# Performance work log

Hardware: AMD Instinct MI355X
Metric: run time of the kernel (lower is better)

The kernel has to match this reference:

```python
import jax, jax.numpy as jnp
import numpy as np
import math

B, S, D, H, L, FF, T = 2, 1024, 1024, 16, 8, 4096, 512
HD = D // H
EPS = 1e-5


def _ln(x, g, b):
    m = jnp.mean(x, axis=-1, keepdims=True)
    v = jnp.var(x, axis=-1, keepdims=True)
    return (x - m) * jax.lax.rsqrt(v + EPS) * g + b


def _rope(x, cos, sin):
    # x: [B,S,H,HD]; interleaved even/odd rotary as in _apply_rotary_emb_sincos
    xe, xo = x[..., 0::2], x[..., 1::2]
    c = cos[None, :, None, :]
    s = sin[None, :, None, :]
    return jnp.stack([xe * c - xo * s, xe * s + xo * c], axis=-1).reshape(x.shape)


def setup_inputs():
    key = jax.random.key(0)
    ks = iter(jax.random.split(key, 40))
    n = lambda shape, sc=0.02: jax.random.normal(next(ks), shape, jnp.float32) * sc
    return {
        "inputs_embeds": jax.random.normal(next(ks), (B, S, D), jnp.float32),
        "attention_mask": jnp.ones((B, 1, 1, S), jnp.float32),
        "time_step": jax.random.uniform(next(ks), (B,), jnp.float32),
        "wpe": n((S, D)),
        "ln1_g": jnp.ones((L, D)), "ln1_b": jnp.zeros((L, D)),
        "attn_w": n((L, D, 3 * D)), "attn_b": jnp.zeros((L, 3 * D)),
        "projw": n((L, D, D)), "projb": jnp.zeros((L, D)),
        "ln2_g": jnp.ones((L, D)), "ln2_b": jnp.zeros((L, D)),
        "fcw": n((L, D, FF)), "fcb": jnp.zeros((L, FF)),
        "pw2": n((L, FF, D)), "pb2": jnp.zeros((L, D)),
        "sst": n((L, 6, D), 1.0 / D ** 0.5),
        "te_w1": n((T, D)), "te_b1": jnp.zeros((D,)),
        "te_w2": n((D, D)), "te_b2": jnp.zeros((D,)),
        "ada_w": n((D, 6 * D)), "ada_b": jnp.zeros((6 * D,)),
        "lnf_g": jnp.ones((D,)), "lnf_b": jnp.zeros((D,)),
        "fsst": n((2, D), 1.0 / D ** 0.5),
        "out_w": n((D, D)), "out_b": jnp.zeros((D,)),
    }


def reference(inputs_embeds, attention_mask, time_step, wpe, ln1_g, ln1_b,
              attn_w, attn_b, projw, projb, ln2_g, ln2_b, fcw, fcb, pw2, pb2,
              sst, te_w1, te_b1, te_w2, te_b2, ada_w, ada_b, lnf_g, lnf_b,
              fsst, out_w, out_b):
    hs = inputs_embeds + wpe[:S][None]  # position embedding
    # rotary tables: [S, HD//2]
    half = HD // 2
    freqs = 1.0 / (10000.0 ** (jnp.arange(half, dtype=jnp.float32) * 2.0 / HD))
    ang = jnp.arange(S, dtype=jnp.float32)[:, None] * freqs[None]
    cos, sin = jnp.cos(ang), jnp.sin(ang)
    mask = (1.0 - attention_mask) * jnp.finfo(jnp.float32).min  # [B,1,1,S]
    # timestep embedding (flow_t_size=T, scale=1000, max_period=10000)
    halfT = T // 2
    tf = jnp.exp(-math.log(10000.0) * jnp.arange(halfT, dtype=jnp.float32) / halfT)
    targs = time_step[:, None] * tf[None] * 1000.0
    tproj = jnp.concatenate([jnp.cos(targs), jnp.sin(targs)], axis=-1)  # [B,T]
    emb = jax.nn.silu(tproj @ te_w1 + te_b1) @ te_w2 + te_b2  # [B,D]
    adaln = (jax.nn.silu(emb) @ ada_w + ada_b).reshape(B, 6, D)

    layer_params = dict(ln1_g=ln1_g, ln1_b=ln1_b, aw=attn_w, ab=attn_b,
                        pw=projw, pb=projb, ln2_g=ln2_g, ln2_b=ln2_b,
                        fw=fcw, fb=fcb, qw=pw2, qb=pb2, sst=sst)

    def block(h, p):
        mod = p["sst"][None] + adaln  # [B,6,D]
        sh1, sc1, g1, sh2, sc2, g2 = [mod[:, i:i + 1] for i in range(6)]
        res = h
        x = _ln(h, p["ln1_g"], p["ln1_b"]) * (1.0 + sc1) + sh1
        qkv = x @ p["aw"] + p["ab"]
        q, k, v = [t.reshape(B, S, H, HD) for t in jnp.split(qkv, 3, axis=-1)]
        q, k = _rope(q, cos, sin), _rope(k, cos, sin)
        scores = jnp.einsum("bqhd,bkhd->bhqk", q, k) / math.sqrt(HD) + mask
        attn = jax.nn.softmax(scores, axis=-1)
        o = jnp.einsum("bhqk,bkhd->bqhd", attn, v).reshape(B, S, D)
        o = o @ p["pw"] + p["pb"]
        h = o * g1 + res
        res = h
        x = _ln(h, p["ln2_g"], p["ln2_b"]) * (1.0 + sc2) + sh2
        x = jax.nn.gelu(x @ p["fw"] + p["fb"], approximate=True) @ p["qw"] + p["qb"]
        return x * g2 + res, None

    hs, _ = jax.lax.scan(block, hs, layer_params)
    fmod = fsst[None] + emb[:, None]  # [B,2,D]
    shift, scale = fmod[:, 0:1], fmod[:, 1:2]
    hs = _ln(hs, lnf_g, lnf_b) * (1.0 + scale) + shift
    return hs @ out_w + out_b
```

## Files before the change

kernel.cpp:

```cpp
#include <hip/hip_runtime.h>
#include <stdint.h>

typedef unsigned short u16;
typedef __attribute__((ext_vector_type(8))) short bf8_t;
typedef __attribute__((ext_vector_type(4))) float f4_t;

#define DEV static __device__ __forceinline__
#define MFMA16(a, b, c) __builtin_amdgcn_mfma_f32_16x16x32_bf16((a), (b), (c), 0, 0, 0)
#define GLDS(gp, lp) __builtin_amdgcn_global_load_lds((const __attribute__((address_space(1))) void*)(gp), \
                                                      (__attribute__((address_space(3))) void*)(lp), 16, 0, 0)

DEV u16 f2bf(float f) {
  union { float f; uint32_t u; } x; x.f = f;
  uint32_t r = x.u + 0x7FFFu + ((x.u >> 16) & 1u);
  return (u16)(r >> 16);
}

DEV void transpose_body(const float* __restrict__ W, u16* __restrict__ WT, int K, int N,
                        int n0, int k0, u16 (*tl)[66]) {
  const int t = threadIdx.x;
  const int tx = t & 15, ty = t >> 4;
  #pragma unroll
  for (int i = 0; i < 64; i += 16) {
    const float4 v = *(const float4*)&W[(long)(k0 + ty + i) * N + n0 + tx * 4];
    tl[tx * 4 + 0][ty + i] = f2bf(v.x);
    tl[tx * 4 + 1][ty + i] = f2bf(v.y);
    tl[tx * 4 + 2][ty + i] = f2bf(v.z);
    tl[tx * 4 + 3][ty + i] = f2bf(v.w);
  }
  __syncthreads();
  const int c = t & 15, r = t >> 4;
  #pragma unroll
  for (int i = 0; i < 64; i += 16) {
    const u16* p = &tl[r + i][c * 4];
    uint2 w;
    w.x = (uint32_t)p[0] | ((uint32_t)p[1] << 16);
    w.y = (uint32_t)p[2] | ((uint32_t)p[3] << 16);
    *(uint2*)&WT[(long)(n0 + r + i) * K + k0 + c * 4] = w;
  }
}

__global__ __launch_bounds__(256) void transpose_k(const float* __restrict__ W, u16* __restrict__ WT,
                                                   int K, int N) {
  __shared__ u16 tl[64][66];
  transpose_body(W, WT, K, N, blockIdx.x * 64, blockIdx.y * 64, tl);
}

__global__ __launch_bounds__(256)
void transpose4_k(const float* __restrict__ w0, u16* __restrict__ o0,
                  const float* __restrict__ w1, u16* __restrict__ o1,
                  const float* __restrict__ w2, u16* __restrict__ o2,
                  const float* __restrict__ w3, u16* __restrict__ o3) {
  __shared__ u16 tl[64][66];
  int bid = blockIdx.x;
  const float* W; u16* O; int K, N, nbx;
  if (bid < 768)        {             W = w0; O = o0; K = 1024; N = 3072; nbx = 48; }
  else if (bid < 1024)  { bid -= 768; W = w1; O = o1; K = 1024; N = 1024; nbx = 16; }
  else if (bid < 2048)  { bid -= 1024; W = w2; O = o2; K = 1024; N = 4096; nbx = 64; }
  else                  { bid -= 2048; W = w3; O = o3; K = 4096; N = 1024; nbx = 16; }
  transpose_body(W, O, K, N, (bid % nbx) * 64, (bid / nbx) * 64, tl);
}

enum { EPI_F32 = 0, EPI_GATE = 1, EPI_GELU = 2, EPI_RAW = 3 };

template <int BM, int EPI, int KS>
__global__ __launch_bounds__(256)
void gemm_bt(const u16* __restrict__ A, const u16* __restrict__ BT, const float* __restrict__ bias,
             float* outF, u16* outB, const float* gate, const float* res, int M, int N, int K) {
  constexpr int MI = BM / 32;
  __shared__ u16 sA[2][BM * 32];
  __shared__ u16 sB[2][128 * 32];
  const int tid = threadIdx.x, lane = tid & 63, wid = tid >> 6;
  const long rowBase = (long)blockIdx.x * BM;
  const long colBase = (long)blockIdx.y * 128;
  const int kz = (KS > 1) ? blockIdx.z : 0;
  const int kbeg = kz * (K / KS);
  const int wr = (wid >> 1) * (BM / 2), wc = (wid & 1) * 64;
  const int fr = lane & 15, kg = (lane >> 4) * 8;

  const f4_t zero = {0.0f, 0.0f, 0.0f, 0.0f};
  f4_t acc[MI][4];
  #pragma unroll
  for (int i = 0; i < MI; ++i)
    #pragma unroll
    for (int j = 0; j < 4; ++j) acc[i][j] = zero;

  const int sr = lane >> 2, scol = (lane & 3) * 8;
  const int c0 = wid * 2;
  const u16 *Ag0, *Ag1 = nullptr, *Bg0, *Bg1;
  int aoff0, aoff1 = 0, boff0, boff1;
  if constexpr (BM == 128) {
    Ag0 = A + (rowBase + c0 * 16 + sr) * (long)K + scol;
    Ag1 = A + (rowBase + c0 * 16 + 16 + sr) * (long)K + scol;
    aoff0 = (c0 * 16) * 32;
    aoff1 = (c0 * 16 + 16) * 32;
  } else {
    Ag0 = A + (rowBase + wid * 16 + sr) * (long)K + scol;
    aoff0 = (wid * 16) * 32;
  }
  Bg0 = BT + (colBase + c0 * 16 + sr) * (long)K + scol;
  Bg1 = BT + (colBase + c0 * 16 + 16 + sr) * (long)K + scol;
  boff0 = (c0 * 16) * 32;
  boff1 = (c0 * 16 + 16) * 32;

  auto stage = [&](int buf, int k0) {
    GLDS(Ag0 + k0, &sA[buf][aoff0]);
    if constexpr (BM == 128) GLDS(Ag1 + k0, &sA[buf][aoff1]);
// ... 9 lines not shown
    if (t + 1 < nk) stage(cur ^ 1, kbeg + (t + 1) * 32);
    bf8_t af[MI], bfv[4];
    #pragma unroll
    for (int m = 0; m < MI; ++m) af[m] = *(const bf8_t*)&sA[cur][(wr + m * 16 + fr) * 32 + kg];
    #pragma unroll
    for (int n = 0; n < 4; ++n) bfv[n] = *(const bf8_t*)&sB[cur][(wc + n * 16 + fr) * 32 + kg];
    #pragma unroll
    for (int m = 0; m < MI; ++m)
      #pragma unroll
      for (int n = 0; n < 4; ++n) acc[m][n] = MFMA16(af[m], bfv[n], acc[m][n]);
    __syncthreads();
    cur ^= 1;
  }

  const int r0 = (lane >> 4) * 4;
  #pragma unroll
  for (int m = 0; m < MI; ++m) {
    #pragma unroll
    for (int n = 0; n < 4; ++n) {
      const long col = colBase + wc + n * 16 + fr;
      const float bv = (EPI == EPI_RAW) ? 0.0f : bias[col];
      #pragma unroll
      for (int j = 0; j < 4; ++j) {
        const long row = rowBase + wr + m * 16 + r0 + j;
        float v = acc[m][n][j] + bv;
        if (EPI == EPI_F32) {
          outF[row * N + col] = v;
        } else if (EPI == EPI_RAW) {
          outF[((long)kz * M + row) * N + col] = v;
        } else if (EPI == EPI_GATE) {
          const int b = (int)(row >> 10);
          const float g = gate[(long)b * 6144 + col];
          outF[row * N + col] = v * g + res[row * N + col];
        } else {
          const float t = 0.7978845608028654f * (v + 0.044715f * v * v * v);
          const float e = __expf(2.0f * t);
          const float th = 1.0f - 2.0f / (e + 1.0f);
          outB[row * N + col] = f2bf(0.5f * v * (1.0f + th));
        }
      }
    }
  }
}

__global__ __launch_bounds__(256)
void ln_mod(const float* __restrict__ h, const float* __restrict__ gamma, const float* __restrict__ beta,
            const float* shp, const float* scp, int bstride, u16* __restrict__ xb) {
  const int row = blockIdx.x * 4 + (threadIdx.x >> 6);
  const int lane = threadIdx.x & 63;
  const int b = row >> 10;
  const long base = (long)row * 1024;
  f4_t x[4];
  float s = 0.0f;
  #pragma unroll
  for (int j = 0; j < 4; ++j) {
    x[j] = *(const f4_t*)&h[base + j * 256 + lane * 4];
    s += x[j][0] + x[j][1] + x[j][2] + x[j][3];
  }
  #pragma unroll
  for (int o = 32; o > 0; o >>= 1) s += __shfl_xor(s, o);
  const float mean = s * 0.0009765625f;
  float vs = 0.0f;
  #pragma unroll
  for (int j = 0; j < 4; ++j)
    #pragma unroll
    for (int e = 0; e < 4; ++e) { const float d = x[j][e] - mean; vs += d * d; }
// ... 37 lines not shown
    f4_t o;
    #pragma unroll
    for (int e = 0; e < 4; ++e) o[e] = (p[e] + q[e] + bv[e]) * gv[e] + r[e];
    *(f4_t*)&hs[base + col] = o;
    v[j] = o;
    s += o[0] + o[1] + o[2] + o[3];
  }
  #pragma unroll
  for (int o = 32; o > 0; o >>= 1) s += __shfl_xor(s, o);
  const float mean = s * 0.0009765625f;
  float vs = 0.0f;
  #pragma unroll
  for (int j = 0; j < 4; ++j)
    #pragma unroll
    for (int e = 0; e < 4; ++e) { const float d = v[j][e] - mean; vs += d * d; }
  #pragma unroll
  for (int o = 32; o > 0; o >>= 1) vs += __shfl_xor(vs, o);
  const float inv = rsqrtf(vs * 0.0009765625f + 1e-5f);
  #pragma unroll
  for (int j = 0; j < 4; ++j) {
    const int col = j * 256 + lane * 4;
    const f4_t gg = *(const f4_t*)&gamma[col];
    const f4_t bb = *(const f4_t*)&beta[col];
    const f4_t sh = *(const f4_t*)&shp[(long)b * bstride + col];
    const f4_t sc = *(const f4_t*)&scp[(long)b * bstride + col];
    union { u16 u[4]; uint2 v; } pk;
    #pragma unroll
    for (int e = 0; e < 4; ++e)
      pk.u[e] = f2bf(((v[j][e] - mean) * inv * gg[e] + bb[e]) * (1.0f + sc[e]) + sh[e]);
    *(uint2*)&xb[base + col] = pk.v;
  }
}

__global__ __launch_bounds__(256)
void rope_split(const float* __restrict__ qkv, const float* __restrict__ ct, const float* __restrict__ st,
                u16* __restrict__ qb, u16* __restrict__ kb) {
  const int row = blockIdx.x;
  const int b = row >> 10, s = row & 1023;
  const float* rp = qkv + (long)row * 3072;
  const int t = threadIdx.x;
  #pragma unroll
  for (int which = 0; which < 2; ++which) {
    const float* xp = rp + which * 1024;
    u16* op = which ? kb : qb;
    #pragma unroll
    for (int j = 0; j < 2; ++j) {
      const int p = t + j * 256;
      const int h = p >> 5, i = p & 31;
      const float2 xx = *(const float2*)&xp[h * 64 + 2 * i];
      const float c = ct[s * 32 + i], sn = st[s * 32 + i];
      const long base = (((long)(b * 16 + h)) * 1024 + s) * 64 + 2 * i;
      const uint32_t w = (uint32_t)f2bf(xx.x * c - xx.y * sn) |
                         ((uint32_t)f2bf(xx.x * sn + xx.y * c) << 16);
      *(uint32_t*)&op[base] = w;
    }
  }
}

__global__ __launch_bounds__(256)
void v_transpose(const float* __restrict__ qkv, u16* __restrict__ vt) {
  __shared__ u16 tl[64][66];
  const int s0 = blockIdx.x * 64;
  const int h = blockIdx.y, b = blockIdx.z;
  const int t = threadIdx.x;
  const int tx = t & 15, ty = t >> 4;
  #pragma unroll
  for (int i = 0; i < 64; i += 16) {
    const float4 v = *(const float4*)&qkv[(long)(b * 1024 + s0 + ty + i) * 3072 + 2048 + h * 64 + tx * 4];
    tl[tx * 4 + 0][ty + i] = f2bf(v.x);
    tl[tx * 4 + 1][ty + i] = f2bf(v.y);
    tl[tx * 4 + 2][ty + i] = f2bf(v.z);
    tl[tx * 4 + 3][ty + i] = f2bf(v.w);
  }
  __syncthreads();
  const int c = t & 15, r = t >> 4;
  #pragma unroll
  for (int i = 0; i < 64; i += 16) {
    const u16* p = &tl[r + i][c * 4];
    uint2 w;
    w.x = (uint32_t)p[0] | ((uint32_t)p[1] << 16);
    w.y = (uint32_t)p[2] | ((uint32_t)p[3] << 16);
    *(uint2*)&vt[((long)(b * 16 + h) * 64 + r + i) * 1024 + s0 + c * 4] = w;
  }
}

DEV void attn_body(bf8_t (&kcur)[4][2], bf8_t (&knxt)[4][2], const bf8_t (&qf)[2],
                   f4_t (&oacc)[4], float& m, float& psum, int kc,
                   const u16* __restrict__ Kp, const u16* __restrict__ Vt,
                   const float* smadd, u16* myP, int fr, int g) {
  const f4_t zero = {0.0f, 0.0f, 0.0f, 0.0f};
  bf8_t vf[4][2];
  #pragma unroll
  for (int dt = 0; dt < 4; ++dt)
    #pragma unroll
    for (int ks = 0; ks < 2; ++ks)
      vf[dt][ks] = *(const bf8_t*)&Vt[(long)(dt * 16 + fr) * 1024 + kc + ks * 32 + g * 8];
  f4_t st[4];
  #pragma unroll
  for (int kt = 0; kt < 4; ++kt) {
    st[kt] = MFMA16(kcur[kt][0], qf[0], zero);
    st[kt] = MFMA16(kcur[kt][1], qf[1], st[kt]);
  }
  {
    const int kn = (kc + 64) & 1023;
    #pragma unroll
    for (int kt = 0; kt < 4; ++kt)
      #pragma unroll
      for (int dh = 0; dh < 2; ++dh)
        knxt[kt][dh] = *(const bf8_t*)&Kp[(long)(kn + kt * 16 + fr) * 64 + dh * 32 + g * 8];
  }
  float p[4][4];
  float cm = -3.402823466e38f;
  #pragma unroll
  for (int kt = 0; kt < 4; ++kt) {
    const f4_t ma = *(const f4_t*)&smadd[kc + kt * 16 + g * 4];
    #pragma unroll
    for (int j = 0; j < 4; ++j) {
      p[kt][j] = st[kt][j] * 0.125f + ma[j];
      cm = fmaxf(cm, p[kt][j]);
    }
  }
  cm = fmaxf(cm, __shfl_xor(cm, 16));
  cm = fmaxf(cm, __shfl_xor(cm, 32));
  const float nm = fmaxf(m, cm);
  const float sc = __expf(m - nm);
  m = nm;
  float ls = 0.0f;
  #pragma unroll
  for (int kt = 0; kt < 4; ++kt)
    #pragma unroll
    for (int j = 0; j < 4; ++j) {
      p[kt][j] = __expf(p[kt][j] - nm);
      ls += p[kt][j];
    }
  psum = psum * sc + ls;
  #pragma unroll
  for (int dt = 0; dt < 4; ++dt)
    #pragma unroll
    for (int j = 0; j < 4; ++j) oacc[dt][j] *= sc;
  #pragma unroll
  for (int kt = 0; kt < 4; ++kt) {
    const int kb = kt * 2 + (g >> 1);
    uint2 w;
    w.x = (uint32_t)f2bf(p[kt][0]) | ((uint32_t)f2bf(p[kt][1]) << 16);
    w.y = (uint32_t)f2bf(p[kt][2]) | ((uint32_t)f2bf(p[kt][3]) << 16);
    *(uint2*)&myP[(kb * 16 + fr) * 8 + (g & 1) * 4] = w;
  }
  bf8_t pa0 = *(const bf8_t*)&myP[(g * 16 + fr) * 8];
  bf8_t pa1 = *(const bf8_t*)&myP[((4 + g) * 16 + fr) * 8];
  #pragma unroll
  for (int dt = 0; dt < 4; ++dt) {
    oacc[dt] = MFMA16(vf[dt][0], pa0, oacc[dt]);
    oacc[dt] = MFMA16(vf[dt][1], pa1, oacc[dt]);
  }
}

__global__ __launch_bounds__(64)
void attn_k(const u16* __restrict__ qb, const u16* __restrict__ kb, const u16* __restrict__ vt,
            const float* __restrict__ amask, u16* __restrict__ ob) {
  __shared__ float smadd[1024];
  __shared__ u16 pl[1024];
  const int q0 = blockIdx.x * 16;
  const int h = blockIdx.y, b = blockIdx.z;
  const long bh = b * 16 + h;
  const int lane = threadIdx.x;
  const int fr = lane & 15, g = lane >> 4;

  #pragma unroll
  for (int i = 0; i < 4; ++i) {
    const int e = (lane + i * 64) * 4;
    const f4_t am = *(const f4_t*)&amask[b * 1024 + e];
    f4_t md;
    #pragma unroll
    for (int j = 0; j < 4; ++j) md[j] = (1.0f - am[j]) * -3.402823466e38f;
    *(f4_t*)&smadd[e] = md;
  }

  const u16* Q = qb + (bh * 1024 + q0) * 64;
  const u16* Kp = kb + bh * 1024 * 64;
  const u16* Vt = vt + bh * 64 * 1024;

  bf8_t qf[2];
  qf[0] = *(const bf8_t*)&Q[fr * 64 + g * 8];
  qf[1] = *(const bf8_t*)&Q[fr * 64 + 32 + g * 8];

  const f4_t zero = {0.0f, 0.0f, 0.0f, 0.0f};
  f4_t oacc[4];
  #pragma unroll
  for (int dt = 0; dt < 4; ++dt) oacc[dt] = zero;
  float m = -1e30f, psum = 0.0f;

  bf8_t kfA[4][2], kfB[4][2];
  #pragma unroll
  for (int kt = 0; kt < 4; ++kt)
    #pragma unroll
    for (int dh = 0; dh < 2; ++dh)
      kfA[kt][dh] = *(const bf8_t*)&Kp[(long)(kt * 16 + fr) * 64 + dh * 32 + g * 8];

  for (int kc = 0; kc < 1024; kc += 128) {
    attn_body(kfA, kfB, qf, oacc, m, psum, kc, Kp, Vt, smadd, pl, fr, g);
    attn_body(kfB, kfA, qf, oacc, m, psum, kc + 64, Kp, Vt, smadd, pl, fr, g);
  }

  float ts = psum + __shfl_xor(psum, 16);
  ts += __shfl_xor(ts, 32);
  const float inv = 1.0f / ts;
  const long qrow = (long)b * 1024 + q0 + fr;
  #pragma unroll
  for (int dt = 0; dt < 4; ++dt) {
    union { u16 u[4]; uint2 v; } pk;
    #pragma unroll
    for (int j = 0; j < 4; ++j) pk.u[j] = f2bf(oacc[dt][j] * inv);
    *(uint2*)&ob[qrow * 1024 + h * 64 + dt * 16 + g * 4] = pk.v;
  }
}

__global__ void rope_tables(float* ct, float* st) {
  const int i = blockIdx.x * 256 + threadIdx.x;
  const int s = i >> 5, k = i & 31;
  const float freq = __expf(-9.210340371976184f * (float)(2 * k) / 64.0f);
  const float a = (float)s * freq;
  ct[i] = cosf(a);
  st[i] = sinf(a);
}

__global__ void init_hs(const float* __restrict__ e, const float* __restrict__ wpe, float* __restrict__ hs) {
  const long i = (long)blockIdx.x * 256 + threadIdx.x;
  float4 a = ((const float4*)e)[i];
  const float4 w = ((const float4*)wpe)[i & 262143];
  a.x += w.x; a.y += w.y; a.z += w.z; a.w += w.w;
  ((float4*)hs)[i] = a;
}

__global__ void time_proj_k(const float* __restrict__ ts, float* __restrict__ tproj) {
  const int j = blockIdx.x * 256 + threadIdx.x;
  const int b = blockIdx.y;
  const float tf = __expf(-9.210340371976184f * (float)(j & 255) / 256.0f);
  const float a = ts[b] * tf * 1000.0f;
  tproj[b * 512 + j] = (j < 256) ? cosf(a) : sinf(a);
}

__global__ __launch_bounds__(256)
void time_mlp1(const float* __restrict__ tproj, const float* __restrict__ w1,
               const float* __restrict__ b1, float* __restrict__ h1) {
  __shared__ float red[8][32];
  const int dl = threadIdx.x & 31, sl = threadIdx.x >> 5;
  const int d = blockIdx.x * 32 + dl, b = blockIdx.y;
  float acc = 0.0f;
  for (int j = sl * 64; j < sl * 64 + 64; ++j) acc += tproj[b * 512 + j] * w1[(long)j * 1024 + d];
  red[sl][dl] = acc;
  __syncthreads();
  if (threadIdx.x < 32) {
    const int dd = blockIdx.x * 32 + threadIdx.x;
    float a = b1[dd];
    #pragma unroll
    for (int s = 0; s < 8; ++s) a += red[s][threadIdx.x];
    h1[b * 1024 + dd] = a / (1.0f + __expf(-a));
  }
}

__global__ __launch_bounds__(256)
void time_mlp2(const float* __restrict__ h1, const float* __restrict__ w2,
               const float* __restrict__ b2, float* __restrict__ emb) {
  __shared__ float red[8][32];
  const int dl = threadIdx.x & 31, sl = threadIdx.x >> 5;
  const int d = blockIdx.x * 32 + dl, b = blockIdx.y;
  float acc = 0.0f;
  for (int j = sl * 128; j < sl * 128 + 128; ++j) acc += h1[b * 1024 + j] * w2[(long)j * 1024 + d];
  red[sl][dl] = acc;
  __syncthreads();
  if (threadIdx.x < 32) {
    const int dd = blockIdx.x * 32 + threadIdx.x;
    float a = b2[dd];
    #pragma unroll
    for (int s = 0; s < 8; ++s) a += red[s][threadIdx.x];
    emb[b * 1024 + dd] = a;
  }
}

__global__ void silu_k(const float* __restrict__ in, float* __restrict__ out, int n) {
  const int i = blockIdx.x * 256 + threadIdx.x;
  if (i < n) { const float v = in[i]; out[i] = v / (1.0f + __expf(-v)); }
}

__global__ void adaln_part(const float* __restrict__ se, const float* __restrict__ aw,
                           float* __restrict__ part) {
  const int j = blockIdx.x * 256 + threadIdx.x;
  const int b = blockIdx.y, kz = blockIdx.z;
  float acc = 0.0f;
  for (int k = kz * 128; k < kz * 128 + 128; ++k) acc += se[b * 1024 + k] * aw[(long)k * 6144 + j];
  part[((long)kz * 2 + b) * 6144 + j] = acc;
}

__global__ void adaln_reduce(const float* __restrict__ part, const float* __restrict__ ab,
                             float* __restrict__ adaln) {
  const int j = blockIdx.x * 256 + threadIdx.x;
  const int b = blockIdx.y;
  float acc = ab[j];
  #pragma unroll
  for (int kz = 0; kz < 8; ++kz) acc += part[((long)kz * 2 + b) * 6144 + j];
  adaln[b * 6144 + j] = acc;
}

__global__ void build_mods(const float* __restrict__ sst, const float* __restrict__ adaln,
                           const float* __restrict__ fsst, const float* __restrict__ emb,
                           float* __restrict__ modAll, float* __restrict__ fmod) {
  const int i = blockIdx.x * 256 + threadIdx.x;
  if (i < 98304) {
    const int d = i & 1023;
    const int rest = i >> 10;
    const int slot = rest % 6;
    const int t2 = rest / 6;
    const int bb = t2 & 1, l = t2 >> 1;
    modAll[i] = sst[(long)(l * 6 + slot) * 1024 + d] + adaln[bb * 6144 + slot * 1024 + d];
  } else if (i < 98304 + 4096) {
    const int j = i - 98304;
    const int d = j & 1023;
    const int slot = (j >> 10) & 1;
    const int bb = j >> 11;
    fmod[j] = fsst[slot * 1024 + d] + emb[bb * 1024 + d];
  }
}

// ... 8 lines not shown
  const float* ln1_b  = (const float*)d_in[5];
  const float* attn_w = (const float*)d_in[6];
  const float* attn_b = (const float*)d_in[7];
  const float* projw  = (const float*)d_in[8];
  const float* projb  = (const float*)d_in[9];
  const float* ln2_g  = (const float*)d_in[10];
  const float* ln2_b  = (const float*)d_in[11];
  const float* fcw    = (const float*)d_in[12];
  const float* fcb    = (const float*)d_in[13];
  const float* pw2    = (const float*)d_in[14];
  const float* pb2    = (const float*)d_in[15];
  const float* sst    = (const float*)d_in[16];
  const float* te_w1  = (const float*)d_in[17];
  const float* te_b1  = (const float*)d_in[18];
  const float* te_w2  = (const float*)d_in[19];
  const float* te_b2  = (const float*)d_in[20];
  const float* ada_w  = (const float*)d_in[21];
  const float* ada_b  = (const float*)d_in[22];
  const float* lnf_g  = (const float*)d_in[23];
  const float* lnf_b  = (const float*)d_in[24];
  const float* fsst   = (const float*)d_in[25];
  const float* out_w  = (const float*)d_in[26];
  const float* out_b  = (const float*)d_in[27];
  float* out = (float*)d_out;
  (void)in_sizes; (void)n_in; (void)out_size; (void)ws_size;

  char* wsb = (char*)d_ws;
  size_t off = 0;
  auto alloc = [&](size_t bytes) -> void* {
    void* p = wsb + off;
    off += (bytes + 255) & ~(size_t)255;
    return p;
  };
  u16* wtA = (u16*)alloc(3072ll * 1024 * 2);
  u16* wtP = (u16*)alloc(1024ll * 1024 * 2);
  u16* wtF = (u16*)alloc(4096ll * 1024 * 2);
  u16* wtQ = (u16*)alloc(1024ll * 4096 * 2);
  u16* wtO = (u16*)alloc(1024ll * 1024 * 2);
  float* hs   = (float*)alloc(2048ll * 1024 * 4);
  float* qkv  = (float*)alloc(2048ll * 3072 * 4);
  u16*   ffb  = (u16*)qkv;
  float* part = (float*)alloc(2ll * 2048 * 1024 * 4);
  u16* xb = (u16*)alloc(2048ll * 1024 * 2);
  u16* qb = (u16*)alloc(2048ll * 1024 * 2);
  u16* kb = (u16*)alloc(2048ll * 1024 * 2);
  u16* vt = (u16*)alloc(2048ll * 1024 * 2);
  u16* ob = (u16*)alloc(2048ll * 1024 * 2);
  float* ct    = (float*)alloc(32768 * 4);
  float* st    = (float*)alloc(32768 * 4);
  float* tproj = (float*)alloc(2 * 512 * 4);
  float* h1    = (float*)alloc(2 * 1024 * 4);
  float* emb   = (float*)alloc(2 * 1024 * 4);
  float* se    = (float*)alloc(2 * 1024 * 4);
  float* adaln = (float*)alloc(2 * 6144 * 4);
  float* modAll = (float*)alloc(8ll * 2 * 6 * 1024 * 4);
  float* fmod   = (float*)alloc(2 * 2 * 1024 * 4);

  rope_tables<<<128, 256, 0, stream>>>(ct, st);
  init_hs<<<2048, 256, 0, stream>>>(inp_emb, wpe, hs);
  time_proj_k<<<dim3(2, 2), 256, 0, stream>>>(tstep, tproj);
  time_mlp1<<<dim3(32, 2), 256, 0, stream>>>(tproj, te_w1, te_b1, h1);
  time_mlp2<<<dim3(32, 2), 256, 0, stream>>>(h1, te_w2, te_b2, emb);
  silu_k<<<8, 256, 0, stream>>>(emb, se, 2048);
  adaln_part<<<dim3(24, 2, 8), 256, 0, stream>>>(se, ada_w, part);
  adaln_reduce<<<dim3(24, 2), 256, 0, stream>>>(part, ada_b, adaln);
  build_mods<<<400, 256, 0, stream>>>(sst, adaln, fsst, emb, modAll, fmod);
  transpose_k<<<dim3(16, 16), 256, 0, stream>>>(out_w, wtO, 1024, 1024);

  ln_mod<<<512, 256, 0, stream>>>(hs, ln1_g, ln1_b, modAll + 0 * 1024, modAll + 1 * 1024, 6144, xb);

  for (int l = 0; l < 8; ++l) {
    const float* ml = modAll + (long)l * 12288;
    transpose4_k<<<3072, 256, 0, stream>>>(attn_w + (long)l * 1024 * 3072, wtA,
                                           projw + (long)l * 1024 * 1024, wtP,
                                           fcw + (long)l * 1024 * 4096, wtF,
                                           pw2 + (long)l * 4096 * 1024, wtQ);

    gemm_bt<128, EPI_F32, 1><<<dim3(16, 24), 256, 0, stream>>>(xb, wtA, attn_b + l * 3072,
                                                               qkv, nullptr, nullptr, nullptr, 2048, 3072, 1024);
    rope_split<<<2048, 256, 0, stream>>>(qkv, ct, st, qb, kb);
    v_transpose<<<dim3(16, 16, 2), 256, 0, stream>>>(qkv, vt);
    attn_k<<<dim3(64, 16, 2), 64, 0, stream>>>(qb, kb, vt, amask, ob);
    gemm_bt<64, EPI_GATE, 1><<<dim3(32, 8), 256, 0, stream>>>(ob, wtP, projb + l * 1024,
                                                              hs, nullptr, ml + 2 * 1024, hs, 2048, 1024, 1024);
    ln_mod<<<512, 256, 0, stream>>>(hs, ln2_g + l * 1024, ln2_b + l * 1024,
                                    ml + 3 * 1024, ml + 4 * 1024, 6144, xb);
    gemm_bt<128, EPI_GELU, 1><<<dim3(16, 32), 256, 0, stream>>>(xb, wtF, fcb + l * 4096,
                                                                nullptr, ffb, nullptr, nullptr, 2048, 4096, 1024);
    gemm_bt<128, EPI_RAW, 2><<<dim3(16, 8, 2), 256, 0, stream>>>(ffb, wtQ, nullptr,
                                                                 part, nullptr, nullptr, nullptr, 2048, 1024, 4096);
    if (l < 7) {
      const float* mln = modAll + (long)(l + 1) * 12288;
      reduce_gate_ln<<<512, 256, 0, stream>>>(part, pb2 + l * 1024, ml + 5 * 1024, hs,
                                              ln1_g + (l + 1) * 1024, ln1_b + (l + 1) * 1024,
                                              mln + 0 * 1024, mln + 1 * 1024, 6144, xb);
    } else {
      reduce_gate_ln<<<512, 256, 0, stream>>>(part, pb2 + l * 1024, ml + 5 * 1024, hs,
                                              lnf_g, lnf_b, fmod + 0, fmod + 1024, 2048, xb);
    }
  }

  gemm_bt<64, EPI_F32, 1><<<dim3(32, 8), 256, 0, stream>>>(xb, wtO, out_b,
                                                           out, nullptr, nullptr, nullptr, 2048, 1024, 1024);
}
```

Baseline: 1.826 ms.

## Split attention over KV halves, batch weight transposes, fuse small prologue kernels

Attention now splits the key/value range into two halves per query tile, which doubles the grid size. A new combine kernel merges the two partial results using their saved max and sum values. All eight layers' weight transposes now run in one launch before the layer loop rather than once per layer. RoPE and the V transpose are fused into one kernel, and time_proj and silu are folded into their consumer kernels. The cost is extra fp32 partial-output traffic and one more kernel per layer, plus larger buffers to hold the transposed weights for every layer.

```diff
diff --git a/kernel.cpp b/kernel.cpp
--- a/kernel.cpp
+++ b/kernel.cpp
@@ -47,17 +47,19 @@
 }
 
 __global__ __launch_bounds__(256)
-void transpose4_k(const float* __restrict__ w0, u16* __restrict__ o0,
-                  const float* __restrict__ w1, u16* __restrict__ o1,
-                  const float* __restrict__ w2, u16* __restrict__ o2,
-                  const float* __restrict__ w3, u16* __restrict__ o3) {
+void transpose_all(const float* __restrict__ attn_w, u16* __restrict__ wtA,
+                   const float* __restrict__ projw, u16* __restrict__ wtP,
+                   const float* __restrict__ fcw, u16* __restrict__ wtF,
+                   const float* __restrict__ pw2, u16* __restrict__ wtQ) {
   __shared__ u16 tl[64][66];
   int bid = blockIdx.x;
+  const int l = bid / 3072;
+  bid -= l * 3072;
   const float* W; u16* O; int K, N, nbx;
-  if (bid < 768)        {             W = w0; O = o0; K = 1024; N = 3072; nbx = 48; }
-  else if (bid < 1024)  { bid -= 768; W = w1; O = o1; K = 1024; N = 1024; nbx = 16; }
-  else if (bid < 2048)  { bid -= 1024; W = w2; O = o2; K = 1024; N = 4096; nbx = 64; }
-  else                  { bid -= 2048; W = w3; O = o3; K = 4096; N = 1024; nbx = 16; }
+  if (bid < 768)        {             W = attn_w + (long)l * 3145728; O = wtA + (long)l * 3145728; K = 1024; N = 3072; nbx = 48; }
+  else if (bid < 1024)  { bid -= 768; W = projw + (long)l * 1048576; O = wtP + (long)l * 1048576; K = 1024; N = 1024; nbx = 16; }
+  else if (bid < 2048)  { bid -= 1024; W = fcw + (long)l * 4194304; O = wtF + (long)l * 4194304; K = 1024; N = 4096; nbx = 64; }
+  else                  { bid -= 2048; W = pw2 + (long)l * 4194304; O = wtQ + (long)l * 4194304; K = 4096; N = 1024; nbx = 16; }
   transpose_body(W, O, K, N, (bid % nbx) * 64, (bid / nbx) * 64, tl);
 }
 
@@ -252,59 +254,52 @@
 }
 
 __global__ __launch_bounds__(256)
-void rope_split(const float* __restrict__ qkv, const float* __restrict__ ct, const float* __restrict__ st,
-                u16* __restrict__ qb, u16* __restrict__ kb) {
-  const int row = blockIdx.x;
-  const int b = row >> 10, s = row & 1023;
-  const float* rp = qkv + (long)row * 3072;
-  const int t = threadIdx.x;
-  #pragma unroll
-  for (int which = 0; which < 2; ++which) {
-    const float* xp = rp + which * 1024;
-    u16* op = which ? kb : qb;
-    #pragma unroll
-    for (int j = 0; j < 2; ++j) {
-      const int p = t + j * 256;
-      const int h = p >> 5, i = p & 31;
-      const float2 xx = *(const float2*)&xp[h * 64 + 2 * i];
-      const float c = ct[s * 32 + i], sn = st[s * 32 + i];
-      const long base = (((long)(b * 16 + h)) * 1024 + s) * 64 + 2 * i;
-      const uint32_t w = (uint32_t)f2bf(xx.x * c - xx.y * sn) |
-                         ((uint32_t)f2bf(xx.x * sn + xx.y * c) << 16);
-      *(uint32_t*)&op[base] = w;
-    }
-  }
-}
-
-__global__ __launch_bounds__(256)
-void v_transpose(const float* __restrict__ qkv, u16* __restrict__ vt) {
+void rope_v(const float* __restrict__ qkv, const float* __restrict__ ct, const float* __restrict__ st,
+            u16* __restrict__ qb, u16* __restrict__ kb, u16* __restrict__ vt) {
   __shared__ u16 tl[64][66];
   const int s0 = blockIdx.x * 64;
   const int h = blockIdx.y, b = blockIdx.z;
+  const long bh = b * 16 + h;
   const int t = threadIdx.x;
+
+  const int i = t & 31, r0 = t >> 5;
+  #pragma unroll
+  for (int which = 0; which < 2; ++which) {
+    u16* op = which ? kb : qb;
+    #pragma unroll
+    for (int it = 0; it < 8; ++it) {
+      const int s = s0 + r0 + it * 8;
+      const float2 xx = *(const float2*)&qkv[(long)(b * 1024 + s) * 3072 + which * 1024 + h * 64 + 2 * i];
+      const float c = ct[s * 32 + i], sn = st[s * 32 + i];
+      const uint32_t w = (uint32_t)f2bf(xx.x * c - xx.y * sn) |
+                         ((uint32_t)f2bf(xx.x * sn + xx.y * c) << 16);
+      *(uint32_t*)&op[(bh * 1024 + s) * 64 + 2 * i] = w;
+    }
+  }
+
   const int tx = t & 15, ty = t >> 4;
   #pragma unroll
-  for (int i = 0; i < 64; i += 16) {
-    const float4 v = *(const float4*)&qkv[(long)(b * 1024 + s0 + ty + i) * 3072 + 2048 + h * 64 + tx * 4];
-    tl[tx * 4 + 0][ty + i] = f2bf(v.x);
-    tl[tx * 4 + 1][ty + i] = f2bf(v.y);
-    tl[tx * 4 + 2][ty + i] = f2bf(v.z);
-    tl[tx * 4 + 3][ty + i] = f2bf(v.w);
+  for (int i2 = 0; i2 < 64; i2 += 16) {
+    const float4 v = *(const float4*)&qkv[(long)(b * 1024 + s0 + ty + i2) * 3072 + 2048 + h * 64 + tx * 4];
+    tl[tx * 4 + 0][ty + i2] = f2bf(v.x);
+    tl[tx * 4 + 1][ty + i2] = f2bf(v.y);
+    tl[tx * 4 + 2][ty + i2] = f2bf(v.z);
+    tl[tx * 4 + 3][ty + i2] = f2bf(v.w);
   }
   __syncthreads();
-  const int c = t & 15, r = t >> 4;
-  #pragma unroll
-  for (int i = 0; i < 64; i += 16) {
-    const u16* p = &tl[r + i][c * 4];
+  const int c2 = t & 15, r2 = t >> 4;
+  #pragma unroll
+  for (int i2 = 0; i2 < 64; i2 += 16) {
+    const u16* p = &tl[r2 + i2][c2 * 4];
     uint2 w;
     w.x = (uint32_t)p[0] | ((uint32_t)p[1] << 16);
     w.y = (uint32_t)p[2] | ((uint32_t)p[3] << 16);
-    *(uint2*)&vt[((long)(b * 16 + h) * 64 + r + i) * 1024 + s0 + c * 4] = w;
+    *(uint2*)&vt[(bh * 64 + r2 + i2) * 1024 + s0 + c2 * 4] = w;
   }
 }
 
 DEV void attn_body(bf8_t (&kcur)[4][2], bf8_t (&knxt)[4][2], const bf8_t (&qf)[2],
-                   f4_t (&oacc)[4], float& m, float& psum, int kc,
+                   f4_t (&oacc)[4], float& m, float& psum, int kc, int kv0,
                    const u16* __restrict__ Kp, const u16* __restrict__ Vt,
                    const float* smadd, u16* myP, int fr, int g) {
   const f4_t zero = {0.0f, 0.0f, 0.0f, 0.0f};
@@ -321,7 +316,7 @@
     st[kt] = MFMA16(kcur[kt][1], qf[1], st[kt]);
   }
   {
-    const int kn = (kc + 64) & 1023;
+    const int kn = kv0 + ((kc - kv0 + 64) & 511);
     #pragma unroll
     for (int kt = 0; kt < 4; ++kt)
       #pragma unroll
@@ -375,12 +370,14 @@
 }
 
 __global__ __launch_bounds__(64)
-void attn_k(const u16* __restrict__ qb, const u16* __restrict__ kb, const u16* __restrict__ vt,
-            const float* __restrict__ amask, u16* __restrict__ ob) {
+void attn_part(const u16* __restrict__ qb, const u16* __restrict__ kb, const u16* __restrict__ vt,
+               const float* __restrict__ amask, float* __restrict__ pO, float2* __restrict__ pml) {
   __shared__ float smadd[1024];
   __shared__ u16 pl[1024];
   const int q0 = blockIdx.x * 16;
-  const int h = blockIdx.y, b = blockIdx.z;
+  const int h = blockIdx.y;
+  const int bz = blockIdx.z, b = bz >> 1, half = bz & 1;
+  const int kv0 = half * 512;
   const long bh = b * 16 + h;
   const int lane = threadIdx.x;
   const int fr = lane & 15, g = lane >> 4;
@@ -414,24 +411,41 @@
   for (int kt = 0; kt < 4; ++kt)
     #pragma unroll
     for (int dh = 0; dh < 2; ++dh)
-      kfA[kt][dh] = *(const bf8_t*)&Kp[(long)(kt * 16 + fr) * 64 + dh * 32 + g * 8];
-
-  for (int kc = 0; kc < 1024; kc += 128) {
-    attn_body(kfA, kfB, qf, oacc, m, psum, kc, Kp, Vt, smadd, pl, fr, g);
-    attn_body(kfB, kfA, qf, oacc, m, psum, kc + 64, Kp, Vt, smadd, pl, fr, g);
+      kfA[kt][dh] = *(const bf8_t*)&Kp[(long)(kv0 + kt * 16 + fr) * 64 + dh * 32 + g * 8];
+
+  for (int kc = kv0; kc < kv0 + 512; kc += 128) {
+    attn_body(kfA, kfB, qf, oacc, m, psum, kc, kv0, Kp, Vt, smadd, pl, fr, g);
+    attn_body(kfB, kfA, qf, oacc, m, psum, kc + 64, kv0, Kp, Vt, smadd, pl, fr, g);
   }
 
   float ts = psum + __shfl_xor(psum, 16);
   ts += __shfl_xor(ts, 32);
-  const float inv = 1.0f / ts;
   const long qrow = (long)b * 1024 + q0 + fr;
-  #pragma unroll
-  for (int dt = 0; dt < 4; ++dt) {
-    union { u16 u[4]; uint2 v; } pk;
-    #pragma unroll
-    for (int j = 0; j < 4; ++j) pk.u[j] = f2bf(oacc[dt][j] * inv);
-    *(uint2*)&ob[qrow * 1024 + h * 64 + dt * 16 + g * 4] = pk.v;
-  }
+  float* pOh = pO + (long)half * 2048 * 1024;
+  #pragma unroll
+  for (int dt = 0; dt < 4; ++dt)
+    *(f4_t*)&pOh[qrow * 1024 + h * 64 + dt * 16 + g * 4] = oacc[dt];
+  if (g == 0)
+    pml[(((long)half * 2 + b) * 16 + h) * 1024 + q0 + fr] = make_float2(m, ts);
+}
+
+__global__ __launch_bounds__(256)
+void attn_combine(const float* __restrict__ pO, const float2* __restrict__ pml, u16* __restrict__ ob) {
+  const int row = blockIdx.x;
+  const int b = row >> 10, s = row & 1023;
+  const int t = threadIdx.x;
+  const int h = t >> 4;
+  const float2 a0 = pml[(((long)0 * 2 + b) * 16 + h) * 1024 + s];
+  const float2 a1 = pml[(((long)1 * 2 + b) * 16 + h) * 1024 + s];
+  const float M = fmaxf(a0.x, a1.x);
+  const float w0 = __expf(a0.x - M), w1 = __expf(a1.x - M);
+  const float inv = 1.0f / (a0.y * w0 + a1.y * w1);
+  const f4_t o0 = *(const f4_t*)&pO[(long)row * 1024 + t * 4];
+  const f4_t o1 = *(const f4_t*)&pO[2048ll * 1024 + (long)row * 1024 + t * 4];
+  union { u16 u[4]; uint2 v; } pk;
+  #pragma unroll
+  for (int j = 0; j < 4; ++j) pk.u[j] = f2bf((o0[j] * w0 + o1[j] * w1) * inv);
+  *(uint2*)&ob[(long)row * 1024 + t * 4] = pk.v;
 }
 
 __global__ void rope_tables(float* ct, float* st) {
@@ -451,22 +465,20 @@
   ((float4*)hs)[i] = a;
 }
 
-__global__ void time_proj_k(const float* __restrict__ ts, float* __restrict__ tproj) {
-  const int j = blockIdx.x * 256 + threadIdx.x;
-  const int b = blockIdx.y;
-  const float tf = __expf(-9.210340371976184f * (float)(j & 255) / 256.0f);
-  const float a = ts[b] * tf * 1000.0f;
-  tproj[b * 512 + j] = (j < 256) ? cosf(a) : sinf(a);
-}
-
-__global__ __launch_bounds__(256)
-void time_mlp1(const float* __restrict__ tproj, const float* __restrict__ w1,
+__global__ __launch_bounds__(256)
+void time_mlp1(const float* __restrict__ ts, const float* __restrict__ w1,
                const float* __restrict__ b1, float* __restrict__ h1) {
   __shared__ float red[8][32];
   const int dl = threadIdx.x & 31, sl = threadIdx.x >> 5;
   const int d = blockIdx.x * 32 + dl, b = blockIdx.y;
+  const float tsv = ts[b];
   float acc = 0.0f;
-  for (int j = sl * 64; j < sl * 64 + 64; ++j) acc += tproj[b * 512 + j] * w1[(long)j * 1024 + d];
+  for (int j = sl * 64; j < sl * 64 + 64; ++j) {
+    const float tf = __expf(-9.210340371976184f * (float)(j & 255) / 256.0f);
+    const float a = tsv * tf * 1000.0f;
+    const float val = (j < 256) ? cosf(a) : sinf(a);
+    acc += val * w1[(long)j * 1024 + d];
+  }
   red[sl][dl] = acc;
   __syncthreads();
   if (threadIdx.x < 32) {
@@ -497,17 +509,15 @@
   }
 }
 
-__global__ void silu_k(const float* __restrict__ in, float* __restrict__ out, int n) {
-  const int i = blockIdx.x * 256 + threadIdx.x;
-  if (i < n) { const float v = in[i]; out[i] = v / (1.0f + __expf(-v)); }
-}
-
-__global__ void adaln_part(const float* __restrict__ se, const float* __restrict__ aw,
+__global__ void adaln_part(const float* __restrict__ emb, const float* __restrict__ aw,
                            float* __restrict__ part) {
   const int j = blockIdx.x * 256 + threadIdx.x;
   const int b = blockIdx.y, kz = blockIdx.z;
   float acc = 0.0f;
-  for (int k = kz * 128; k < kz * 128 + 128; ++k) acc += se[b * 1024 + k] * aw[(long)k * 6144 + j];
+  for (int k = kz * 128; k < kz * 128 + 128; ++k) {
+    const float e = emb[b * 1024 + k];
+    acc += (e / (1.0f + __expf(-e))) * aw[(long)k * 6144 + j];
+  }
   part[((long)kz * 2 + b) * 6144 + j] = acc;
 }
 
@@ -582,15 +592,17 @@
     off += (bytes + 255) & ~(size_t)255;
     return p;
   };
-  u16* wtA = (u16*)alloc(3072ll * 1024 * 2);
-  u16* wtP = (u16*)alloc(1024ll * 1024 * 2);
-  u16* wtF = (u16*)alloc(4096ll * 1024 * 2);
-  u16* wtQ = (u16*)alloc(1024ll * 4096 * 2);
+  u16* wtA = (u16*)alloc(8ll * 3072 * 1024 * 2);
+  u16* wtP = (u16*)alloc(8ll * 1024 * 1024 * 2);
+  u16* wtF = (u16*)alloc(8ll * 4096 * 1024 * 2);
+  u16* wtQ = (u16*)alloc(8ll * 1024 * 4096 * 2);
   u16* wtO = (u16*)alloc(1024ll * 1024 * 2);
   float* hs   = (float*)alloc(2048ll * 1024 * 4);
   float* qkv  = (float*)alloc(2048ll * 3072 * 4);
   u16*   ffb  = (u16*)qkv;
   float* part = (float*)alloc(2ll * 2048 * 1024 * 4);
+  float* pO   = (float*)alloc(2ll * 2048 * 1024 * 4);
+  float2* pml = (float2*)alloc(2ll * 2 * 16 * 1024 * 8);
   u16* xb = (u16*)alloc(2048ll * 1024 * 2);
   u16* qb = (u16*)alloc(2048ll * 1024 * 2);
   u16* kb = (u16*)alloc(2048ll * 1024 * 2);
@@ -598,46 +610,38 @@
   u16* ob = (u16*)alloc(2048ll * 1024 * 2);
   float* ct    = (float*)alloc(32768 * 4);
   float* st    = (float*)alloc(32768 * 4);
-  float* tproj = (float*)alloc(2 * 512 * 4);
   float* h1    = (float*)alloc(2 * 1024 * 4);
   float* emb   = (float*)alloc(2 * 1024 * 4);
-  float* se    = (float*)alloc(2 * 1024 * 4);
   float* adaln = (float*)alloc(2 * 6144 * 4);
   float* modAll = (float*)alloc(8ll * 2 * 6 * 1024 * 4);
   float* fmod   = (float*)alloc(2 * 2 * 1024 * 4);
 
   rope_tables<<<128, 256, 0, stream>>>(ct, st);
   init_hs<<<2048, 256, 0, stream>>>(inp_emb, wpe, hs);
-  time_proj_k<<<dim3(2, 2), 256, 0, stream>>>(tstep, tproj);
-  time_mlp1<<<dim3(32, 2), 256, 0, stream>>>(tproj, te_w1, te_b1, h1);
+  time_mlp1<<<dim3(32, 2), 256, 0, stream>>>(tstep, te_w1, te_b1, h1);
   time_mlp2<<<dim3(32, 2), 256, 0, stream>>>(h1, te_w2, te_b2, emb);
-  silu_k<<<8, 256, 0, stream>>>(emb, se, 2048);
-  adaln_part<<<dim3(24, 2, 8), 256, 0, stream>>>(se, ada_w, part);
+  adaln_part<<<dim3(24, 2, 8), 256, 0, stream>>>(emb, ada_w, part);
   adaln_reduce<<<dim3(24, 2), 256, 0, stream>>>(part, ada_b, adaln);
   build_mods<<<400, 256, 0, stream>>>(sst, adaln, fsst, emb, modAll, fmod);
   transpose_k<<<dim3(16, 16), 256, 0, stream>>>(out_w, wtO, 1024, 1024);
+  transpose_all<<<8 * 3072, 256, 0, stream>>>(attn_w, wtA, projw, wtP, fcw, wtF, pw2, wtQ);
 
   ln_mod<<<512, 256, 0, stream>>>(hs, ln1_g, ln1_b, modAll + 0 * 1024, modAll + 1 * 1024, 6144, xb);
 
   for (int l = 0; l < 8; ++l) {
     const float* ml = modAll + (long)l * 12288;
-    transpose4_k<<<3072, 256, 0, stream>>>(attn_w + (long)l * 1024 * 3072, wtA,
-                                           projw + (long)l * 1024 * 1024, wtP,
-                                           fcw + (long)l * 1024 * 4096, wtF,
-                                           pw2 + (long)l * 4096 * 1024, wtQ);
-
-    gemm_bt<128, EPI_F32, 1><<<dim3(16, 24), 256, 0, stream>>>(xb, wtA, attn_b + l * 3072,
+    gemm_bt<128, EPI_F32, 1><<<dim3(16, 24), 256, 0, stream>>>(xb, wtA + (long)l * 3145728, attn_b + l * 3072,
                                                                qkv, nullptr, nullptr, nullptr, 2048, 3072, 1024);
-    rope_split<<<2048, 256, 0, stream>>>(qkv, ct, st, qb, kb);
-    v_transpose<<<dim3(16, 16, 2), 256, 0, stream>>>(qkv, vt);
-    attn_k<<<dim3(64, 16, 2), 64, 0, stream>>>(qb, kb, vt, amask, ob);
-    gemm_bt<64, EPI_GATE, 1><<<dim3(32, 8), 256, 0, stream>>>(ob, wtP, projb + l * 1024,
+    rope_v<<<dim3(16, 16, 2), 256, 0, stream>>>(qkv, ct, st, qb, kb, vt);
+    attn_part<<<dim3(64, 16, 4), 64, 0, stream>>>(qb, kb, vt, amask, pO, pml);
+    attn_combine<<<2048, 256, 0, stream>>>(pO, pml, ob);
+    gemm_bt<64, EPI_GATE, 1><<<dim3(32, 8), 256, 0, stream>>>(ob, wtP + (long)l * 1048576, projb + l * 1024,
                                                               hs, nullptr, ml + 2 * 1024, hs, 2048, 1024, 1024);
     ln_mod<<<512, 256, 0, stream>>>(hs, ln2_g + l * 1024, ln2_b + l * 1024,
                                     ml + 3 * 1024, ml + 4 * 1024, 6144, xb);
-    gemm_bt<128, EPI_GELU, 1><<<dim3(16, 32), 256, 0, stream>>>(xb, wtF, fcb + l * 4096,
+    gemm_bt<128, EPI_GELU, 1><<<dim3(16, 32), 256, 0, stream>>>(xb, wtF + (long)l * 4194304, fcb + l * 4096,
                                                                 nullptr, ffb, nullptr, nullptr, 2048, 4096, 1024);
-    gemm_bt<128, EPI_RAW, 2><<<dim3(16, 8, 2), 256, 0, stream>>>(ffb, wtQ, nullptr,
+    gemm_bt<128, EPI_RAW, 2><<<dim3(16, 8, 2), 256, 0, stream>>>(ffb, wtQ + (long)l * 4194304, nullptr,
                                                                  part, nullptr, nullptr, nullptr, 2048, 1024, 4096);
     if (l < 7) {
       const float* mln = modAll + (long)(l + 1) * 12288;
```

After: 2.115 ms. 15.9% more time.

## Fuse RoPE and V transpose into QKV GEMM epilogue; remap GEMM blocks across XCDs

Applied to the files above, without the earlier changes.

The QKV GEMM epilogue now applies RoPE, getting the pair partner through a lane shuffle, and writes bf16 Q/K plus transposed V directly. This removes the fp32 qkv buffer and the separate rope_split and v_transpose kernels. All GEMMs switch to a 1D grid with an XCD-aware block swizzle meant to improve L2 locality. Small time-embedding kernels (time_proj, silu) are folded into their consumers to cut launches. The V-transposed stores from the epilogue are strided scalar writes, which may coalesce poorly.

```diff
diff --git a/kernel.cpp b/kernel.cpp
--- a/kernel.cpp
+++ b/kernel.cpp
@@ -61,18 +61,24 @@
   transpose_body(W, O, K, N, (bid % nbx) * 64, (bid / nbx) * 64, tl);
 }
 
-enum { EPI_F32 = 0, EPI_GATE = 1, EPI_GELU = 2, EPI_RAW = 3 };
+enum { EPI_F32 = 0, EPI_GATE = 1, EPI_GELU = 2, EPI_RAW = 3, EPI_QKV = 4 };
 
 template <int BM, int EPI, int KS>
 __global__ __launch_bounds__(256)
 void gemm_bt(const u16* __restrict__ A, const u16* __restrict__ BT, const float* __restrict__ bias,
-             float* outF, u16* outB, const float* gate, const float* res, int M, int N, int K) {
+             float* outF, u16* outB, const float* gate, const float* res,
+             u16* kbuf, u16* vtbuf, int M, int N, int K) {
   constexpr int MI = BM / 32;
   __shared__ u16 sA[2][BM * 32];
   __shared__ u16 sB[2][128 * 32];
   const int tid = threadIdx.x, lane = tid & 63, wid = tid >> 6;
-  const long rowBase = (long)blockIdx.x * BM;
-  const long colBase = (long)blockIdx.y * 128;
+
+  int wg = blockIdx.x;
+  { const int q = gridDim.x >> 3; wg = (wg & 7) * q + (wg >> 3); }
+  const int nbx = M / BM;
+  const long rowBase = (long)(wg % nbx) * BM;
+  const long colBase = (long)(wg / nbx) * 128;
+
   const int kz = (KS > 1) ? blockIdx.z : 0;
   const int kbeg = kz * (K / KS);
   const int wr = (wid >> 1) * (BM / 2), wc = (wid & 1) * 64;
@@ -148,6 +154,23 @@
           const int b = (int)(row >> 10);
           const float g = gate[(long)b * 6144 + col];
           outF[row * N + col] = v * g + res[row * N + col];
+        } else if (EPI == EPI_QKV) {
+          const int type = (int)(colBase >> 10);
+          const int cc = (int)(col & 1023);
+          const int hh = cc >> 6, dd = cc & 63;
+          const int b = (int)(row >> 10), spos = (int)(row & 1023);
+          const long bh = (long)b * 16 + hh;
+          const float part = __shfl_xor(v, 1);
+          if (type == 2) {
+            vtbuf[(bh * 64 + dd) * 1024 + spos] = f2bf(v);
+          } else {
+            const int i = dd >> 1;
+            const float c = gate[spos * 32 + i];
+            const float sn = res[spos * 32 + i];
+            const float o = (dd & 1) ? (part * sn + v * c) : (v * c - part * sn);
+            u16* dst = (type == 0) ? outB : kbuf;
+            dst[(bh * 1024 + spos) * 64 + dd] = f2bf(o);
+          }
         } else {
           const float t = 0.7978845608028654f * (v + 0.044715f * v * v * v);
           const float e = __expf(2.0f * t);
@@ -251,58 +274,6 @@
   }
 }
 
-__global__ __launch_bounds__(256)
-void rope_split(const float* __restrict__ qkv, const float* __restrict__ ct, const float* __restrict__ st,
-                u16* __restrict__ qb, u16* __restrict__ kb) {
-  const int row = blockIdx.x;
-  const int b = row >> 10, s = row & 1023;
-  const float* rp = qkv + (long)row * 3072;
-  const int t = threadIdx.x;
-  #pragma unroll
-  for (int which = 0; which < 2; ++which) {
-    const float* xp = rp + which * 1024;
-    u16* op = which ? kb : qb;
-    #pragma unroll
-    for (int j = 0; j < 2; ++j) {
-      const int p = t + j * 256;
-      const int h = p >> 5, i = p & 31;
-      const float2 xx = *(const float2*)&xp[h * 64 + 2 * i];
-      const float c = ct[s * 32 + i], sn = st[s * 32 + i];
-      const long base = (((long)(b * 16 + h)) * 1024 + s) * 64 + 2 * i;
-      const uint32_t w = (uint32_t)f2bf(xx.x * c - xx.y * sn) |
-                         ((uint32_t)f2bf(xx.x * sn + xx.y * c) << 16);
-      *(uint32_t*)&op[base] = w;
-    }
-  }
-}
-
-__global__ __launch_bounds__(256)
-void v_transpose(const float* __restrict__ qkv, u16* __restrict__ vt) {
-  __shared__ u16 tl[64][66];
-  const int s0 = blockIdx.x * 64;
-  const int h = blockIdx.y, b = blockIdx.z;
-  const int t = threadIdx.x;
-  const int tx = t & 15, ty = t >> 4;
-  #pragma unroll
-  for (int i = 0; i < 64; i += 16) {
-    const float4 v = *(const float4*)&qkv[(long)(b * 1024 + s0 + ty + i) * 3072 + 2048 + h * 64 + tx * 4];
-    tl[tx * 4 + 0][ty + i] = f2bf(v.x);
-    tl[tx * 4 + 1][ty + i] = f2bf(v.y);
-    tl[tx * 4 + 2][ty + i] = f2bf(v.z);
-    tl[tx * 4 + 3][ty + i] = f2bf(v.w);
-  }
-  __syncthreads();
-  const int c = t & 15, r = t >> 4;
-  #pragma unroll
-  for (int i = 0; i < 64; i += 16) {
-    const u16* p = &tl[r + i][c * 4];
-    uint2 w;
-    w.x = (uint32_t)p[0] | ((uint32_t)p[1] << 16);
-    w.y = (uint32_t)p[2] | ((uint32_t)p[3] << 16);
-    *(uint2*)&vt[((long)(b * 16 + h) * 64 + r + i) * 1024 + s0 + c * 4] = w;
-  }
-}
-
 DEV void attn_body(bf8_t (&kcur)[4][2], bf8_t (&knxt)[4][2], const bf8_t (&qf)[2],
                    f4_t (&oacc)[4], float& m, float& psum, int kc,
                    const u16* __restrict__ Kp, const u16* __restrict__ Vt,
@@ -451,22 +422,20 @@
   ((float4*)hs)[i] = a;
 }
 
-__global__ void time_proj_k(const float* __restrict__ ts, float* __restrict__ tproj) {
-  const int j = blockIdx.x * 256 + threadIdx.x;
-  const int b = blockIdx.y;
-  const float tf = __expf(-9.210340371976184f * (float)(j & 255) / 256.0f);
-  const float a = ts[b] * tf * 1000.0f;
-  tproj[b * 512 + j] = (j < 256) ? cosf(a) : sinf(a);
-}
-
 __global__ __launch_bounds__(256)
-void time_mlp1(const float* __restrict__ tproj, const float* __restrict__ w1,
+void time_mlp1(const float* __restrict__ ts, const float* __restrict__ w1,
                const float* __restrict__ b1, float* __restrict__ h1) {
   __shared__ float red[8][32];
   const int dl = threadIdx.x & 31, sl = threadIdx.x >> 5;
   const int d = blockIdx.x * 32 + dl, b = blockIdx.y;
+  const float tsv = ts[b];
   float acc = 0.0f;
-  for (int j = sl * 64; j < sl * 64 + 64; ++j) acc += tproj[b * 512 + j] * w1[(long)j * 1024 + d];
+  for (int j = sl * 64; j < sl * 64 + 64; ++j) {
+    const float tf = __expf(-9.210340371976184f * (float)(j & 255) / 256.0f);
+    const float a = tsv * tf * 1000.0f;
+    const float val = (j < 256) ? cosf(a) : sinf(a);
+    acc += val * w1[(long)j * 1024 + d];
+  }
   red[sl][dl] = acc;
   __syncthreads();
   if (threadIdx.x < 32) {
@@ -497,17 +466,15 @@
   }
 }
 
-__global__ void silu_k(const float* __restrict__ in, float* __restrict__ out, int n) {
-  const int i = blockIdx.x * 256 + threadIdx.x;
-  if (i < n) { const float v = in[i]; out[i] = v / (1.0f + __expf(-v)); }
-}
-
-__global__ void adaln_part(const float* __restrict__ se, const float* __restrict__ aw,
+__global__ void adaln_part(const float* __restrict__ emb, const float* __restrict__ aw,
                            float* __restrict__ part) {
   const int j = blockIdx.x * 256 + threadIdx.x;
   const int b = blockIdx.y, kz = blockIdx.z;
   float acc = 0.0f;
-  for (int k = kz * 128; k < kz * 128 + 128; ++k) acc += se[b * 1024 + k] * aw[(long)k * 6144 + j];
+  for (int k = kz * 128; k < kz * 128 + 128; ++k) {
+    const float e = emb[b * 1024 + k];
+    acc += (e / (1.0f + __expf(-e))) * aw[(long)k * 6144 + j];
+  }
   part[((long)kz * 2 + b) * 6144 + j] = acc;
 }
 
@@ -588,8 +555,7 @@
   u16* wtQ = (u16*)alloc(1024ll * 4096 * 2);
   u16* wtO = (u16*)alloc(1024ll * 1024 * 2);
   float* hs   = (float*)alloc(2048ll * 1024 * 4);
-  float* qkv  = (float*)alloc(2048ll * 3072 * 4);
-  u16*   ffb  = (u16*)qkv;
+  u16* ffb    = (u16*)alloc(2048ll * 4096 * 2);
   float* part = (float*)alloc(2ll * 2048 * 1024 * 4);
   u16* xb = (u16*)alloc(2048ll * 1024 * 2);
   u16* qb = (u16*)alloc(2048ll * 1024 * 2);
@@ -598,21 +564,17 @@
   u16* ob = (u16*)alloc(2048ll * 1024 * 2);
   float* ct    = (float*)alloc(32768 * 4);
   float* st    = (float*)alloc(32768 * 4);
-  float* tproj = (float*)alloc(2 * 512 * 4);
   float* h1    = (float*)alloc(2 * 1024 * 4);
   float* emb   = (float*)alloc(2 * 1024 * 4);
-  float* se    = (float*)alloc(2 * 1024 * 4);
   float* adaln = (float*)alloc(2 * 6144 * 4);
   float* modAll = (float*)alloc(8ll * 2 * 6 * 1024 * 4);
   float* fmod   = (float*)alloc(2 * 2 * 1024 * 4);
 
   rope_tables<<<128, 256, 0, stream>>>(ct, st);
   init_hs<<<2048, 256, 0, stream>>>(inp_emb, wpe, hs);
-  time_proj_k<<<dim3(2, 2), 256, 0, stream>>>(tstep, tproj);
-  time_mlp1<<<dim3(32, 2), 256, 0, stream>>>(tproj, te_w1, te_b1, h1);
+  time_mlp1<<<dim3(32, 2), 256, 0, stream>>>(tstep, te_w1, te_b1, h1);
   time_mlp2<<<dim3(32, 2), 256, 0, stream>>>(h1, te_w2, te_b2, emb);
-  silu_k<<<8, 256, 0, stream>>>(emb, se, 2048);
-  adaln_part<<<dim3(24, 2, 8), 256, 0, stream>>>(se, ada_w, part);
+  adaln_part<<<dim3(24, 2, 8), 256, 0, stream>>>(emb, ada_w, part);
   adaln_reduce<<<dim3(24, 2), 256, 0, stream>>>(part, ada_b, adaln);
   build_mods<<<400, 256, 0, stream>>>(sst, adaln, fsst, emb, modAll, fmod);
   transpose_k<<<dim3(16, 16), 256, 0, stream>>>(out_w, wtO, 1024, 1024);
@@ -626,19 +588,20 @@
                                            fcw + (long)l * 1024 * 4096, wtF,
                                            pw2 + (long)l * 4096 * 1024, wtQ);
 
-    gemm_bt<128, EPI_F32, 1><<<dim3(16, 24), 256, 0, stream>>>(xb, wtA, attn_b + l * 3072,
-                                                               qkv, nullptr, nullptr, nullptr, 2048, 3072, 1024);
-    rope_split<<<2048, 256, 0, stream>>>(qkv, ct, st, qb, kb);
-    v_transpose<<<dim3(16, 16, 2), 256, 0, stream>>>(qkv, vt);
+    gemm_bt<128, EPI_QKV, 1><<<384, 256, 0, stream>>>(xb, wtA, attn_b + l * 3072,
+                                                      nullptr, qb, ct, st, kb, vt, 2048, 3072, 1024);
     attn_k<<<dim3(64, 16, 2), 64, 0, stream>>>(qb, kb, vt, amask, ob);
-    gemm_bt<64, EPI_GATE, 1><<<dim3(32, 8), 256, 0, stream>>>(ob, wtP, projb + l * 1024,
-                                                              hs, nullptr, ml + 2 * 1024, hs, 2048, 1024, 1024);
+    gemm_bt<64, EPI_GATE, 1><<<256, 256, 0, stream>>>(ob, wtP, projb + l * 1024,
+                                                      hs, nullptr, ml + 2 * 1024, hs, nullptr, nullptr,
+                                                      2048, 1024, 1024);
     ln_mod<<<512, 256, 0, stream>>>(hs, ln2_g + l * 1024, ln2_b + l * 1024,
                                     ml + 3 * 1024, ml + 4 * 1024, 6144, xb);
-    gemm_bt<128, EPI_GELU, 1><<<dim3(16, 32), 256, 0, stream>>>(xb, wtF, fcb + l * 4096,
-                                                                nullptr, ffb, nullptr, nullptr, 2048, 4096, 1024);
-    gemm_bt<128, EPI_RAW, 2><<<dim3(16, 8, 2), 256, 0, stream>>>(ffb, wtQ, nullptr,
-                                                                 part, nullptr, nullptr, nullptr, 2048, 1024, 4096);
+    gemm_bt<128, EPI_GELU, 1><<<512, 256, 0, stream>>>(xb, wtF, fcb + l * 4096,
+                                                       nullptr, ffb, nullptr, nullptr, nullptr, nullptr,
+                                                       2048, 4096, 1024);
+    gemm_bt<128, EPI_RAW, 2><<<dim3(128, 1, 2), 256, 0, stream>>>(ffb, wtQ, nullptr,
+                                                                  part, nullptr, nullptr, nullptr, nullptr, nullptr,
+                                                                  2048, 1024, 4096);
     if (l < 7) {
       const float* mln = modAll + (long)(l + 1) * 12288;
       reduce_gate_ln<<<512, 256, 0, stream>>>(part, pb2 + l * 1024, ml + 5 * 1024, hs,
@@ -650,6 +613,7 @@
     }
   }
 
-  gemm_bt<64, EPI_F32, 1><<<dim3(32, 8), 256, 0, stream>>>(xb, wtO, out_b,
-                                                           out, nullptr, nullptr, nullptr, 2048, 1024, 1024);
-}
+  gemm_bt<64, EPI_F32, 1><<<256, 256, 0, stream>>>(xb, wtO, out_b,
+                                                   out, nullptr, nullptr, nullptr, nullptr, nullptr,
+                                                   2048, 1024, 1024);
+}
```

After: 1.910 ms. 1.05x slower.
